# Optimization experiments

Measured on AMD Instinct MI355X. Metric: run time of the kernel, lower is better.

The kernel has to match this reference:

```python
import jax, jax.numpy as jnp
import numpy as np

N = 4096
D = 512   # d_model == dff (required by the original code path)
H = 4
NEG = -1e10
ALPHA = 0.3  # keras LeakyReLU default alpha


def setup_inputs() -> dict:
    key = jax.random.key(0)
    ks = jax.random.split(key, 8)
    nodes = jax.random.normal(ks[0], (N, D), dtype=jnp.float32)
    # sparse-ish 0/1 dense adjacency with self loops
    adj = (jax.random.uniform(ks[1], (N, N)) < 0.01).astype(jnp.float32)
    adj = jnp.maximum(adj, jnp.eye(N, dtype=jnp.float32))
    s = 0.05
    W_node = jax.random.normal(ks[2], (D, D), dtype=jnp.float32) * s
    b_node = jnp.zeros((D,), dtype=jnp.float32)
    K = jax.random.normal(ks[3], (H, D, D), dtype=jnp.float32) * s
    A_self = jax.random.normal(ks[4], (H, D), dtype=jnp.float32) * s
    A_neigh = jax.random.normal(ks[5], (H, D), dtype=jnp.float32) * s
    return {"nodes": nodes, "adj": adj, "W_node": W_node, "b_node": b_node,
            "K": K, "A_self": A_self, "A_neigh": A_neigh, "num_heads": H}


def reference(nodes, adj, W_node, b_node, K, A_self, A_neigh, num_heads):
    # node_layer: Dense(dff)
    x = nodes @ W_node + b_node                       # [N, D]
    # per-head projection, vectorized over heads
    feats = jnp.einsum('nd,hdf->hnf', x, K)           # [H, N, D]
    # additive attention scores; both terms are per-row scalars -> [H, N]
    s = jnp.einsum('hnf,hf->hn', feats, A_self) + jnp.einsum('hnf,hf->hn', feats, A_neigh)
    s = jnp.where(s > 0, s, ALPHA * s)                # LeakyReLU(alpha=0.3)
    # broadcast row score over columns + adjacency mask, softmax over neighbors
    logits = s[:, :, None] + NEG * (1.0 - adj)[None]  # [H, N, N]
    attn = jax.nn.softmax(logits, axis=-1)
    # dropout is identity at inference (training=False)
    out = jnp.einsum('hij,hjf->hif', attn, feats)     # [H, N, D]
    out = jnp.mean(out, axis=0)                       # mean over heads
    return jax.nn.relu(out)
```

## Files before the change

### kernel.cpp

```cpp
#include <hip/hip_runtime.h>


typedef short  short8 __attribute__((ext_vector_type(8)));
typedef float  f32x4  __attribute__((ext_vector_type(4)));

__device__ inline unsigned short f2bf(float f) {
    union { float f; unsigned int u; } v; v.f = f;
    unsigned int u = v.u;
    u += 0x7fffu + ((u >> 16) & 1u);
    return (unsigned short)(u >> 16);
}

__device__ inline void gl_lds16(const void* gp, void* lp) {
    __builtin_amdgcn_global_load_lds(
        (const __attribute__((address_space(1))) void*)gp,
        (__attribute__((address_space(3))) void*)lp, 16, 0, 0);
}

__global__ __launch_bounds__(512, 4) void prep_kernel(
        const float* __restrict__ nodes, const float* __restrict__ adj,
        const float* __restrict__ W, const float* __restrict__ b,
        const float* __restrict__ K,
        unsigned short* __restrict__ MmatT, float* __restrict__ bias2,
        unsigned short* __restrict__ nodesBf,
        int* __restrict__ degArr, int* __restrict__ nbrArr,
        int N, int D, int H, int numCast) {
    __shared__ union {
        struct {
            unsigned short As[2][64][40];
            unsigned short Bs[2][64][40];
        } g;
        float red64[64][64];
        int   lst[1024];
    } sm;
    __shared__ float red2[8][64];
    __shared__ int cnt;

    const int bid = blockIdx.x;
    const int tid = threadIdx.x;
    const int DD  = D * D;
    const int lane = tid & 63, wave = tid >> 6;
    const int l15 = lane & 15, quad = lane >> 4;

    if (bid < 64) {
        const int by = bid >> 3, bx = bid & 7;
        const int f0 = by * 64, d0 = bx * 64;
        const float invH = 1.0f / (float)H;
        const int h  = tid >> 8;
        const int th = tid & 255;
        const int wy = (wave >> 1) & 1, wx = wave & 1;
        const int kk = th >> 3;
        const int ff = (th & 7) * 8;
        const int dr = th >> 2;
        const int dk = (th & 3) * 8;
        const int kh = h * 256;

        f32x4 acc[2][2] = {};
        for (int k0 = 0; k0 < 256; k0 += 32) {
            f32x4 kv[4][2];
#pragma unroll
            for (int hh = 0; hh < 4; ++hh) {
                const float* kp = K + ((size_t)hh * D + (kh + k0 + kk)) * D + f0 + ff;
                kv[hh][0] = *reinterpret_cast<const f32x4*>(kp);
                kv[hh][1] = *reinterpret_cast<const f32x4*>(kp + 4);
            }
            const float* wp = W + (size_t)(d0 + dr) * D + kh + k0 + dk;
            f32x4 wu = *reinterpret_cast<const f32x4*>(wp);
            f32x4 wv = *reinterpret_cast<const f32x4*>(wp + 4);

            float s[8];
#pragma unroll
            for (int j = 0; j < 4; ++j) {
                s[j]     = kv[0][0][j] + kv[1][0][j] + kv[2][0][j] + kv[3][0][j];
                s[j + 4] = kv[0][1][j] + kv[1][1][j] + kv[2][1][j] + kv[3][1][j];
            }
            short8 bv;
#pragma unroll
            for (int j = 0; j < 4; ++j) {
                bv[j]     = (short)f2bf(wu[j]);
                bv[j + 4] = (short)f2bf(wv[j]);
            }
            __syncthreads();
#pragma unroll
            for (int j = 0; j < 8; ++j)
                sm.g.As[h][ff + j][kk] = f2bf(s[j] * invH);
            *reinterpret_cast<short8*>(&sm.g.Bs[h][dr][dk]) = bv;
            __syncthreads();
            short8 a0 = *reinterpret_cast<const short8*>(&sm.g.As[h][wy * 32 +      l15][quad * 8]);
            short8 a1 = *reinterpret_cast<const short8*>(&sm.g.As[h][wy * 32 + 16 + l15][quad * 8]);
            short8 b0 = *reinterpret_cast<const short8*>(&sm.g.Bs[h][wx * 32 +      l15][quad * 8]);
            short8 b1 = *reinterpret_cast<const short8*>(&sm.g.Bs[h][wx * 32 + 16 + l15][quad * 8]);
            acc[0][0] = __builtin_amdgcn_mfma_f32_16x16x32_bf16(a0, b0, acc[0][0], 0, 0, 0);
            acc[0][1] = __builtin_amdgcn_mfma_f32_16x16x32_bf16(a0, b1, acc[0][1], 0, 0, 0);
            acc[1][0] = __builtin_amdgcn_mfma_f32_16x16x32_bf16(a1, b0, acc[1][0], 0, 0, 0);
            acc[1][1] = __builtin_amdgcn_mfma_f32_16x16x32_bf16(a1, b1, acc[1][1], 0, 0, 0);
        }
        __syncthreads();
        if (h == 1) {
#pragma unroll
            for (int mi = 0; mi < 2; ++mi)
#pragma unroll
                for (int ni = 0; ni < 2; ++ni)
#pragma unroll
                    for (int r = 0; r < 4; ++r)
                        sm.red64[wy * 32 + mi * 16 + quad * 4 + r]
                                [wx * 32 + ni * 16 + l15] = acc[mi][ni][r];
        }
        __syncthreads();
        if (h == 0) {
#pragma unroll
            for (int mi = 0; mi < 2; ++mi)
#pragma unroll
                for (int ni = 0; ni < 2; ++ni) {
                    int col = d0 + wx * 32 + ni * 16 + l15;
#pragma unroll
                    for (int r = 0; r < 4; ++r) {
                        int row = f0 + wy * 32 + mi * 16 + quad * 4 + r;
                        float v = acc[mi][ni][r] +
                            sm.red64[wy * 32 + mi * 16 + quad * 4 + r]
                                    [wx * 32 + ni * 16 + l15];
                        MmatT[(size_t)row * D + col] = f2bf(v);
                    }
                }
        }
    } else if (bid < 72) {
        const int f0 = (bid - 64) * 64;
        const int fl = tid & 63, grp = tid >> 6;
        const float invH = 1.0f / (float)H;
        float a = 0.f;
        for (int d0i = grp * 64; d0i < grp * 64 + 64; d0i += 4) {
            float v[4] = {0.f, 0.f, 0.f, 0.f};
#pragma unroll
            for (int dd = 0; dd < 4; ++dd)
#pragma unroll
                for (int hh = 0; hh < 4; ++hh)
                    v[dd] += K[((size_t)hh * D + d0i + dd) * D + f0 + fl];
#pragma unroll
            for (int dd = 0; dd < 4; ++dd) a += b[d0i + dd] * v[dd];
        }
        red2[grp][fl] = a;
        __syncthreads();
        if (tid < 64) {
            float s = 0.f;
#pragma unroll
            for (int gg = 0; gg < 8; ++gg) s += red2[gg][tid];
            bias2[f0 + tid] = s * invH;
        }
    } else if (bid < 72 + N) {
        const int row = bid - 72;
        if (tid == 0) cnt = 0;
        __syncthreads();
        const f32x4* ap = reinterpret_cast<const f32x4*>(adj + (size_t)row * N + tid * 8);
        f32x4 av[2];
        av[0] = ap[0];
        av[1] = ap[1];
#pragma unroll
        for (int c = 0; c < 2; ++c) {
            int b4 = tid * 8 + c * 4;
#pragma unroll
            for (int j = 0; j < 4; ++j)
                if (av[c][j] > 0.5f) {
                    int p = atomicAdd(&cnt, 1);
                    if (p < 1024) sm.lst[p] = b4 + j;
                }
        }
        __syncthreads();
        int deg = cnt; if (deg > 1024) deg = 1024;
        if (tid == 0) degArr[row] = deg;
        for (int i = tid; i < deg; i += 512)
            nbrArr[(size_t)row * 1024 + i] = sm.lst[i];
    } else {
        const int total  = (N * D) >> 3;
        const int stride = numCast << 9;
        for (int i = (bid - 72 - N) * 512 + tid; i < total; i += stride) {
            const float* p = nodes + (size_t)i * 8;
            f32x4 x = *reinterpret_cast<const f32x4*>(p);
            f32x4 y = *reinterpret_cast<const f32x4*>(p + 4);
            short8 o;
#pragma unroll
            for (int j = 0; j < 4; ++j) {
                o[j]     = (short)f2bf(x[j]);
                o[j + 4] = (short)f2bf(y[j]);
            }
            *reinterpret_cast<short8*>(nodesBf + (size_t)i * 8) = o;
        }
    }
}

__global__ __launch_bounds__(512) void gemm2_kernel(
        const unsigned short* __restrict__ nodesBf,
        const unsigned short* __restrict__ MmatT,
        const float* __restrict__ bias2, unsigned short* __restrict__ g, int D) {
    __shared__ unsigned short As[2][64][32];
    __shared__ unsigned short Bs[2][64][32];
    const int bid = blockIdx.x;
    const int lb = (bid & 7) * 64 + (bid >> 3);
    const int by = lb >> 3, bx = lb & 7;
    const int tid = threadIdx.x;
    const int lane = tid & 63, wave = tid >> 6;
    const int wy = wave >> 2, wx = wave & 3;
    const int l15 = lane & 15, quad = lane >> 4;

    const int st  = tid & 255;
    const int cgl = ((st & 3) ^ ((st >> 3) & 3)) * 8;
    const unsigned short* Gp = (tid < 256)
        ? nodesBf + (size_t)(by * 64 + (st >> 2)) * D + cgl
        : MmatT   + (size_t)(bx * 64 + (st >> 2)) * D + cgl;
    unsigned short* S0 = (tid < 256)
        ? (&As[0][0][0] + wave * 512)
        : (&Bs[0][0][0] + (wave - 4) * 512);
    unsigned short* S1 = (tid < 256)
        ? (&As[1][0][0] + wave * 512)
        : (&Bs[1][0][0] + (wave - 4) * 512);

    const int ra = wy * 32 + l15;
    const int rb = wx * 16 + l15;
    const int qa = (quad ^ ((ra >> 1) & 3)) * 8;
    const int qb = (quad ^ ((rb >> 1) & 3)) * 8;

    f32x4 acc[2] = {};
    gl_lds16(Gp, S0);

    int cur = 0;
#pragma unroll
    for (int k0 = 0; k0 < 512; k0 += 32) {
        if (k0 + 32 < 512) {
            gl_lds16(Gp + k0 + 32, cur ? S0 : S1);
            asm volatile("s_waitcnt vmcnt(1)" ::: "memory");
        } else {
            asm volatile("s_waitcnt vmcnt(0)" ::: "memory");
        }
        __builtin_amdgcn_s_barrier();
        __builtin_amdgcn_sched_barrier(0);
        const unsigned short* Af = cur ? &As[1][0][0] : &As[0][0][0];
        const unsigned short* Bf = cur ? &Bs[1][0][0] : &Bs[0][0][0];
        short8 a0 = *reinterpret_cast<const short8*>(Af + (ra     ) * 32 + qa);
        short8 a1 = *reinterpret_cast<const short8*>(Af + (ra + 16) * 32 + qa);
        short8 b0 = *reinterpret_cast<const short8*>(Bf + (rb     ) * 32 + qb);
        acc[0] = __builtin_amdgcn_mfma_f32_16x16x32_bf16(a0, b0, acc[0], 0, 0, 0);
        acc[1] = __builtin_amdgcn_mfma_f32_16x16x32_bf16(a1, b0, acc[1], 0, 0, 0);
        __builtin_amdgcn_sched_barrier(0);
        asm volatile("s_waitcnt lgkmcnt(0)" ::: "memory");
        __builtin_amdgcn_s_barrier();
        cur ^= 1;
    }

    {
        const int col = bx * 64 + wx * 16 + l15;
        const float bvl = bias2[col];
#pragma unroll
        for (int mi = 0; mi < 2; ++mi)
#pragma unroll
            for (int r = 0; r < 4; ++r) {
                int row = by * 64 + wy * 32 + mi * 16 + quad * 4 + r;
                g[(size_t)row * D + col] = f2bf(acc[mi][r] + bvl);
            }
    }
}

__global__ __launch_bounds__(256) void aggregate_kernel(
        const int* __restrict__ degArr, const int* __restrict__ nbrArr,
        const unsigned short* __restrict__ g, float* __restrict__ out,
        int N, int D) {
    const int row = blockIdx.x;
    const int tid = threadIdx.x;
    __shared__ int lst[1024];
    const int deg = degArr[row];
    for (int i = tid; i < deg; i += 256) lst[i] = nbrArr[(size_t)row * 1024 + i];
    __syncthreads();

    const int col = tid * 2;
    float acc0 = 0.f, acc1 = 0.f;
    int k = 0;
    for (; k + 8 <= deg; k += 8) {
        unsigned int u[8];
#pragma unroll
        for (int j = 0; j < 8; ++j)
            u[j] = *reinterpret_cast<const unsigned int*>(&g[(size_t)lst[k + j] * D + col]);
#pragma unroll
        for (int j = 0; j < 8; ++j) {
            union { unsigned int i; float f; } lo, hi;
            lo.i = u[j] << 16; hi.i = u[j] & 0xffff0000u;
            acc0 += lo.f; acc1 += hi.f;
        }
    }
    for (; k < deg; ++k) {
        unsigned int u = *reinterpret_cast<const unsigned int*>(&g[(size_t)lst[k] * D + col]);
        union { unsigned int i; float f; } lo, hi;
        lo.i = u << 16; hi.i = u & 0xffff0000u;
        acc0 += lo.f; acc1 += hi.f;
    }

    float inv = deg > 0 ? 1.f / (float)deg : 0.f;
    acc0 *= inv; acc1 *= inv;
    float2 o;
    o.x = acc0 > 0.f ? acc0 : 0.f;
    o.y = acc1 > 0.f ? acc1 : 0.f;
    *reinterpret_cast<float2*>(&out[(size_t)row * D + col]) = o;
}

extern "C" void kernel_launch(void* const* d_in, const int* in_sizes, int n_in,
                              void* d_out, int out_size, void* d_ws, size_t ws_size,
                              hipStream_t stream) {
    const float* nodes  = (const float*)d_in[0];
    const float* adj    = (const float*)d_in[1];
    const float* W_node = (const float*)d_in[2];
    const float* b_node = (const float*)d_in[3];
    const float* K      = (const float*)d_in[4];

    const int D  = in_sizes[3];
    const int N  = in_sizes[0] / D;
    const int H  = in_sizes[4] / (D * D);
    const int DD = D * D;

    float* out = (float*)d_out;

    char* ws = (char*)d_ws;
    unsigned short* MmatT   = (unsigned short*)(ws);
    size_t off = (size_t)DD * 2;
    float*          bias2   = (float*)(ws + off);          off += (size_t)D * 4;
    unsigned short* nodesBf = (unsigned short*)(ws + off); off += (size_t)N * D * 2;
    unsigned short* g_bf16  = (unsigned short*)(ws + off); off += (size_t)N * D * 2;
    int*            degArr  = (int*)(ws + off);            off += (size_t)N * 4;
    int*            nbrArr  = (int*)(ws + off);

    const int numCast = 512;
    prep_kernel<<<dim3(64 + 8 + N + numCast), 512, 0, stream>>>(
        nodes, adj, W_node, b_node, K, MmatT, bias2, nodesBf, degArr, nbrArr,
        N, D, H, numCast);

    gemm2_kernel<<<dim3((N / 64) * (D / 64)), 512, 0, stream>>>(
        nodesBf, MmatT, bias2, g_bf16, D);

    aggregate_kernel<<<dim3(N), 256, 0, stream>>>(degArr, nbrArr, g_bf16, out, N, D);
}
```

Measured before the change: 146.1 us.

## Aggregate raw node rows before the projection GEMM and fuse ReLU into GEMM

Uses linearity to reorder the computation: each row first averages its neighbours' fp32 node rows in the adjacency-scan block, then the averaged bf16 matrix is multiplied by the folded projection matrix with bias and ReLU in the epilogue. This removes the separate bf16 cast pass, the neighbour list and degree writes to global memory, the intermediate g buffer, and one kernel launch. In exchange the gather now reads fp32 rows at twice the bytes per element and sits inside the prep kernel, and bias is added after averaging, which only matches because the rows are row-normalised.

```diff
diff --git a/kernel.cpp b/kernel.cpp
--- a/kernel.cpp
+++ b/kernel.cpp
@@ -22,9 +22,8 @@
         const float* __restrict__ W, const float* __restrict__ b,
         const float* __restrict__ K,
         unsigned short* __restrict__ MmatT, float* __restrict__ bias2,
-        unsigned short* __restrict__ nodesBf,
-        int* __restrict__ degArr, int* __restrict__ nbrArr,
-        int N, int D, int H, int numCast) {
+        unsigned short* __restrict__ aggBf,
+        int N, int D, int H) {
     __shared__ union {
         struct {
             unsigned short As[2][64][40];
@@ -146,7 +145,7 @@
             for (int gg = 0; gg < 8; ++gg) s += red2[gg][tid];
             bias2[f0 + tid] = s * invH;
         }
-    } else if (bid < 72 + N) {
+    } else {
         const int row = bid - 72;
         if (tid == 0) cnt = 0;
         __syncthreads();
@@ -166,31 +165,29 @@
         }
         __syncthreads();
         int deg = cnt; if (deg > 1024) deg = 1024;
-        if (tid == 0) degArr[row] = deg;
-        for (int i = tid; i < deg; i += 512)
-            nbrArr[(size_t)row * 1024 + i] = sm.lst[i];
-    } else {
-        const int total  = (N * D) >> 3;
-        const int stride = numCast << 9;
-        for (int i = (bid - 72 - N) * 512 + tid; i < total; i += stride) {
-            const float* p = nodes + (size_t)i * 8;
-            f32x4 x = *reinterpret_cast<const f32x4*>(p);
-            f32x4 y = *reinterpret_cast<const f32x4*>(p + 4);
-            short8 o;
-#pragma unroll
-            for (int j = 0; j < 4; ++j) {
-                o[j]     = (short)f2bf(x[j]);
-                o[j + 4] = (short)f2bf(y[j]);
-            }
-            *reinterpret_cast<short8*>(nodesBf + (size_t)i * 8) = o;
-        }
+
+        float acc = 0.f;
+        int k = 0;
+        for (; k + 8 <= deg; k += 8) {
+            float u[8];
+#pragma unroll
+            for (int j = 0; j < 8; ++j)
+                u[j] = nodes[(size_t)sm.lst[k + j] * D + tid];
+#pragma unroll
+            for (int j = 0; j < 8; ++j) acc += u[j];
+        }
+        for (; k < deg; ++k)
+            acc += nodes[(size_t)sm.lst[k] * D + tid];
+
+        float inv = 1.f / (float)deg;
+        aggBf[(size_t)row * D + tid] = f2bf(acc * inv);
     }
 }
 
-__global__ __launch_bounds__(512) void gemm2_kernel(
-        const unsigned short* __restrict__ nodesBf,
+__global__ __launch_bounds__(512) void outgemm_kernel(
+        const unsigned short* __restrict__ aggBf,
         const unsigned short* __restrict__ MmatT,
-        const float* __restrict__ bias2, unsigned short* __restrict__ g, int D) {
+        const float* __restrict__ bias2, float* __restrict__ out, int D) {
     __shared__ unsigned short As[2][64][32];
     __shared__ unsigned short Bs[2][64][32];
     const int bid = blockIdx.x;
@@ -204,8 +201,8 @@
     const int st  = tid & 255;
     const int cgl = ((st & 3) ^ ((st >> 3) & 3)) * 8;
     const unsigned short* Gp = (tid < 256)
-        ? nodesBf + (size_t)(by * 64 + (st >> 2)) * D + cgl
-        : MmatT   + (size_t)(bx * 64 + (st >> 2)) * D + cgl;
+        ? aggBf + (size_t)(by * 64 + (st >> 2)) * D + cgl
+        : MmatT + (size_t)(bx * 64 + (st >> 2)) * D + cgl;
     unsigned short* S0 = (tid < 256)
         ? (&As[0][0][0] + wave * 512)
         : (&Bs[0][0][0] + (wave - 4) * 512);
@@ -253,50 +250,10 @@
 #pragma unroll
             for (int r = 0; r < 4; ++r) {
                 int row = by * 64 + wy * 32 + mi * 16 + quad * 4 + r;
-                g[(size_t)row * D + col] = f2bf(acc[mi][r] + bvl);
+                float v = acc[mi][r] + bvl;
+                out[(size_t)row * D + col] = v > 0.f ? v : 0.f;
             }
     }
-}
-
-__global__ __launch_bounds__(256) void aggregate_kernel(
-        const int* __restrict__ degArr, const int* __restrict__ nbrArr,
-        const unsigned short* __restrict__ g, float* __restrict__ out,
-        int N, int D) {
-    const int row = blockIdx.x;
-    const int tid = threadIdx.x;
-    __shared__ int lst[1024];
-    const int deg = degArr[row];
-    for (int i = tid; i < deg; i += 256) lst[i] = nbrArr[(size_t)row * 1024 + i];
-    __syncthreads();
-
-    const int col = tid * 2;
-    float acc0 = 0.f, acc1 = 0.f;
-    int k = 0;
-    for (; k + 8 <= deg; k += 8) {
-        unsigned int u[8];
-#pragma unroll
-        for (int j = 0; j < 8; ++j)
-            u[j] = *reinterpret_cast<const unsigned int*>(&g[(size_t)lst[k + j] * D + col]);
-#pragma unroll
-        for (int j = 0; j < 8; ++j) {
-            union { unsigned int i; float f; } lo, hi;
-            lo.i = u[j] << 16; hi.i = u[j] & 0xffff0000u;
-            acc0 += lo.f; acc1 += hi.f;
-        }
-    }
-    for (; k < deg; ++k) {
-        unsigned int u = *reinterpret_cast<const unsigned int*>(&g[(size_t)lst[k] * D + col]);
-        union { unsigned int i; float f; } lo, hi;
-        lo.i = u << 16; hi.i = u & 0xffff0000u;
-        acc0 += lo.f; acc1 += hi.f;
-    }
-
-    float inv = deg > 0 ? 1.f / (float)deg : 0.f;
-    acc0 *= inv; acc1 *= inv;
-    float2 o;
-    o.x = acc0 > 0.f ? acc0 : 0.f;
-    o.y = acc1 > 0.f ? acc1 : 0.f;
-    *reinterpret_cast<float2*>(&out[(size_t)row * D + col]) = o;
 }
 
 extern "C" void kernel_launch(void* const* d_in, const int* in_sizes, int n_in,
@@ -316,21 +273,14 @@
     float* out = (float*)d_out;
 
     char* ws = (char*)d_ws;
-    unsigned short* MmatT   = (unsigned short*)(ws);
+    unsigned short* MmatT = (unsigned short*)(ws);
     size_t off = (size_t)DD * 2;
-    float*          bias2   = (float*)(ws + off);          off += (size_t)D * 4;
-    unsigned short* nodesBf = (unsigned short*)(ws + off); off += (size_t)N * D * 2;
-    unsigned short* g_bf16  = (unsigned short*)(ws + off); off += (size_t)N * D * 2;
-    int*            degArr  = (int*)(ws + off);            off += (size_t)N * 4;
-    int*            nbrArr  = (int*)(ws + off);
-
-    const int numCast = 512;
-    prep_kernel<<<dim3(64 + 8 + N + numCast), 512, 0, stream>>>(
-        nodes, adj, W_node, b_node, K, MmatT, bias2, nodesBf, degArr, nbrArr,
-        N, D, H, numCast);
-
-    gemm2_kernel<<<dim3((N / 64) * (D / 64)), 512, 0, stream>>>(
-        nodesBf, MmatT, bias2, g_bf16, D);
-
-    aggregate_kernel<<<dim3(N), 256, 0, stream>>>(degArr, nbrArr, g_bf16, out, N, D);
-}
+    float*          bias2 = (float*)(ws + off);          off += (size_t)D * 4;
+    unsigned short* aggBf = (unsigned short*)(ws + off);
+
+    prep_kernel<<<dim3(64 + 8 + N), 512, 0, stream>>>(
+        nodes, adj, W_node, b_node, K, MmatT, bias2, aggBf, N, D, H);
+
+    outgemm_kernel<<<dim3((N / 64) * (D / 64)), 512, 0, stream>>>(
+        aggBf, MmatT, bias2, out, D);
+}
```

Result: slower. 157.7 us (+7.9%).
